# Kernel optimization log

Measured on AMD Instinct MI355X. Metric: run time of the kernel, lower is better.

Reference implementation:

```python
import jax, jax.numpy as jnp
import numpy as np

N = 262144
HIDDEN = 512
NUM_GATES = 64
NUM_GRAPHS = 1024
EPS = 1e-16


def setup_inputs() -> dict:
    key = jax.random.key(0)
    k1, k2, k3 = jax.random.split(key, 3)
    x = jax.random.normal(k1, (N, HIDDEN), dtype=jnp.float32)
    batch = jnp.sort(jax.random.randint(k2, (N,), 0, NUM_GRAPHS, dtype=jnp.int64))
    # Xavier-uniform init for the gate weight [hidden, num_gates]
    limit = float(np.sqrt(6.0 / (HIDDEN + NUM_GATES)))
    W = jax.random.uniform(k3, (HIDDEN, NUM_GATES), dtype=jnp.float32,
                           minval=-limit, maxval=limit)
    return {"x": x, "batch": batch, "W": W}


def _segment_softmax(gate, batch, num_segments):
    # Numerically-stable softmax within each segment (per gate column).
    seg_max = jax.ops.segment_max(gate, batch, num_segments=num_segments)  # [G, num_gates]
    gate = jnp.exp(gate - seg_max[batch])
    seg_sum = jax.ops.segment_sum(gate, batch, num_segments=num_segments)  # [G, num_gates]
    return gate / (seg_sum[batch] + EPS)


def reference(x, batch, W):
    # gate = x @ W : [N, num_gates]
    gate = x @ W
    gate = _segment_softmax(gate, batch, NUM_GRAPHS)
    # weighted scatter-add pooling: out[g] = sum_{i in g} mean_k(gate[i,k]) * x[i]
    weights = jnp.mean(gate, axis=-1, keepdims=True)  # [N, 1]
    out = jax.ops.segment_sum(weights * x, batch, num_segments=NUM_GRAPHS)  # [G, hidden]
    return out
```

## Files before the change

kernel.cpp:

```cpp
#include <hip/hip_runtime.h>

#define NROWS   262144
#define HIDDEN  512
#define NGATES  64
#define NGRAPHS 1024
#define CHUNK   512

typedef __attribute__((ext_vector_type(8))) short short8;
typedef __attribute__((ext_vector_type(4))) float floatx4;

__device__ __forceinline__ unsigned short f2bf(float f) {
    unsigned int u = __float_as_uint(f);
    unsigned int r = (u + 0x7fffu + ((u >> 16) & 1u)) >> 16;
    return (unsigned short)r;
}

__global__ void k_wfrag(const float* __restrict__ W, unsigned short* __restrict__ wf) {
    int tile = blockIdx.x;
    int lane = threadIdx.x;
    int kstep = tile >> 2, nt = tile & 3;
    int kbase = kstep * 32 + (lane >> 4) * 8;
    int col   = nt * 16 + (lane & 15);
    unsigned short* dst = wf + ((size_t)tile * 64 + lane) * 8;
#pragma unroll
    for (int j = 0; j < 8; ++j)
        dst[j] = f2bf(W[(size_t)(kbase + j) * NGATES + col]);
}

__global__ void k_bounds(const int* __restrict__ batch, int* __restrict__ segstart) {
    int g = blockIdx.x * blockDim.x + threadIdx.x;
    if (g > NGRAPHS) return;
    if (g == NGRAPHS) { segstart[g] = NROWS; return; }
    int lo = 0, hi = NROWS;
    while (lo < hi) { int mid = (lo + hi) >> 1; if (batch[mid] < g) lo = mid + 1; else hi = mid; }
    segstart[g] = lo;
}

__global__ __launch_bounds__(256) void k_gemm(const float* __restrict__ x,
                                              const unsigned short* __restrict__ wf,
                                              float* __restrict__ gate) {
    const int t = threadIdx.x;
    const int lane = t & 63, wv = t >> 6;
    const int rowbase = (blockIdx.x * 4 + wv) * 16;
    const int m = lane & 15, q = lane >> 4;
    const float* xrow = x + (size_t)(rowbase + m) * HIDDEN + q * 8;
    const short8* wfv = (const short8*)wf;

    floatx4 acc0 = {0.f,0.f,0.f,0.f}, acc1 = {0.f,0.f,0.f,0.f};
    floatx4 acc2 = {0.f,0.f,0.f,0.f}, acc3 = {0.f,0.f,0.f,0.f};

#pragma unroll 4
    for (int ks = 0; ks < 16; ++ks) {
        float4 a0 = *(const float4*)(xrow + ks * 32);
        float4 a1 = *(const float4*)(xrow + ks * 32 + 4);
        short8 af;
        af[0] = (short)f2bf(a0.x); af[1] = (short)f2bf(a0.y);
        af[2] = (short)f2bf(a0.z); af[3] = (short)f2bf(a0.w);
        af[4] = (short)f2bf(a1.x); af[5] = (short)f2bf(a1.y);
        af[6] = (short)f2bf(a1.z); af[7] = (short)f2bf(a1.w);
        short8 b0 = wfv[(ks * 4 + 0) * 64 + lane];
        short8 b1 = wfv[(ks * 4 + 1) * 64 + lane];
        short8 b2 = wfv[(ks * 4 + 2) * 64 + lane];
        short8 b3 = wfv[(ks * 4 + 3) * 64 + lane];
        acc0 = __builtin_amdgcn_mfma_f32_16x16x32_bf16(af, b0, acc0, 0, 0, 0);
        acc1 = __builtin_amdgcn_mfma_f32_16x16x32_bf16(af, b1, acc1, 0, 0, 0);
        acc2 = __builtin_amdgcn_mfma_f32_16x16x32_bf16(af, b2, acc2, 0, 0, 0);
        acc3 = __builtin_amdgcn_mfma_f32_16x16x32_bf16(af, b3, acc3, 0, 0, 0);
    }

    const int orow = rowbase + q * 4;
    float* gbase = gate + (size_t)orow * NGATES + m;
#pragma unroll
    for (int r = 0; r < 4; ++r) {
        gbase[r * NGATES +  0] = acc0[r];
        gbase[r * NGATES + 16] = acc1[r];
        gbase[r * NGATES + 32] = acc2[r];
        gbase[r * NGATES + 48] = acc3[r];
    }
}

__global__ __launch_bounds__(256) void k_pool(const float* __restrict__ x,
                                              const float* __restrict__ gate,
                                              const int* __restrict__ segstart,
                                              float* __restrict__ out) {
    __shared__ float red[4 * 64];
    __shared__ float mk[64];
    __shared__ float rinv[64];
    __shared__ float wl[CHUNK];

    const int g = blockIdx.x;
    const int t = threadIdx.x;
    const int lane = t & 63, wv = t >> 6;
    const int s = segstart[g], e = segstart[g + 1];

    float mloc = -3.402823466e38f;
    for (int i = s + wv; i < e; i += 4)
        mloc = fmaxf(mloc, gate[(size_t)i * NGATES + lane]);
    red[wv * 64 + lane] = mloc;
    __syncthreads();
    if (t < 64)
        mk[t] = fmaxf(fmaxf(red[t], red[64 + t]), fmaxf(red[128 + t], red[192 + t]));
    __syncthreads();

    const float mkk = mk[lane];
    float sloc = 0.f;
    for (int i = s + wv; i < e; i += 4)
        sloc += __expf(gate[(size_t)i * NGATES + lane] - mkk);
    red[wv * 64 + lane] = sloc;
    __syncthreads();
    if (t < 64)
        rinv[t] = 1.0f / (red[t] + red[64 + t] + red[128 + t] + red[192 + t] + 1e-16f);
    __syncthreads();

    const float rk = rinv[lane];
    const int h0 = t * 2;
    float accx = 0.f, accy = 0.f;

    for (int cbase = s; cbase < e; cbase += CHUNK) {
        const int cn = min(CHUNK, e - cbase);
        for (int i = wv; i < cn; i += 4) {
            const int row = cbase + i;
            float ev = __expf(gate[(size_t)row * NGATES + lane] - mkk) * rk;
#pragma unroll
            for (int off = 32; off >= 1; off >>= 1)
                ev += __shfl_xor(ev, off, 64);
            if (lane == 0) wl[i] = ev * (1.0f / 64.0f);
        }
        __syncthreads();
        for (int i = 0; i < cn; ++i) {
            const float w = wl[i];
            const float2 xv = *(const float2*)(x + (size_t)(cbase + i) * HIDDEN + h0);
            accx = fmaf(w, xv.x, accx);
            accy = fmaf(w, xv.y, accy);
        }
        __syncthreads();
    }

    float2 o; o.x = accx; o.y = accy;
    *(float2*)(out + (size_t)g * HIDDEN + h0) = o;
}

extern "C" void kernel_launch(void* const* d_in, const int* in_sizes, int n_in,
                              void* d_out, int out_size, void* d_ws, size_t ws_size,
                              hipStream_t stream) {
    const float* x     = (const float*)d_in[0];
    const int*   batch = (const int*)d_in[1];
    const float* W     = (const float*)d_in[2];
    float* out = (float*)d_out;

    unsigned short* wfrag = (unsigned short*)d_ws;
    int* segstart = (int*)((char*)d_ws + (64 << 10));
    float* gate   = (float*)((char*)d_ws + (72 << 10));

    hipLaunchKernelGGL(k_wfrag, dim3(64), dim3(64), 0, stream, W, wfrag);
    hipLaunchKernelGGL(k_bounds, dim3(5), dim3(256), 0, stream, batch, segstart);
    hipLaunchKernelGGL(k_gemm, dim3(NROWS / 64), dim3(256), 0, stream, x, wfrag, gate);
    hipLaunchKernelGGL(k_pool, dim3(NGRAPHS), dim3(256), 0, stream, x, gate, segstart, out);
}
```

Measured before the change: 874.1 us.

## Fuse exp and segment-sum into gate GEMM, store bf16 exp, drop max pass

```diff
diff --git a/kernel.cpp b/kernel.cpp
--- a/kernel.cpp
+++ b/kernel.cpp
@@ -13,6 +13,9 @@
     unsigned int u = __float_as_uint(f);
     unsigned int r = (u + 0x7fffu + ((u >> 16) & 1u)) >> 16;
     return (unsigned short)r;
+}
+__device__ __forceinline__ float bf2f(unsigned short u) {
+    return __uint_as_float((unsigned int)u << 16);
 }
 
 __global__ void k_wfrag(const float* __restrict__ W, unsigned short* __restrict__ wf) {
@@ -27,18 +30,24 @@
         dst[j] = f2bf(W[(size_t)(kbase + j) * NGATES + col]);
 }
 
-__global__ void k_bounds(const int* __restrict__ batch, int* __restrict__ segstart) {
-    int g = blockIdx.x * blockDim.x + threadIdx.x;
-    if (g > NGRAPHS) return;
-    if (g == NGRAPHS) { segstart[g] = NROWS; return; }
-    int lo = 0, hi = NROWS;
-    while (lo < hi) { int mid = (lo + hi) >> 1; if (batch[mid] < g) lo = mid + 1; else hi = mid; }
-    segstart[g] = lo;
-}
-
-__global__ __launch_bounds__(256) void k_gemm(const float* __restrict__ x,
+__global__ void k_init(const int* __restrict__ batch, int* __restrict__ segstart,
+                       float* __restrict__ sums) {
+    int tid = blockIdx.x * blockDim.x + threadIdx.x;
+    if (tid < NGRAPHS * NGATES) sums[tid] = 0.f;
+    if (tid <= NGRAPHS) {
+        if (tid == NGRAPHS) { segstart[tid] = NROWS; return; }
+        int lo = 0, hi = NROWS;
+        while (lo < hi) { int mid = (lo + hi) >> 1; if (batch[mid] < tid) lo = mid + 1; else hi = mid; }
+        segstart[tid] = lo;
+    }
+}
+
+__global__ __launch_bounds__(256) void k_gate(const float* __restrict__ x,
                                               const unsigned short* __restrict__ wf,
-                                              float* __restrict__ gate) {
+                                              const int* __restrict__ batch,
+                                              unsigned short* __restrict__ eout,
+                                              float* __restrict__ sums) {
+    __shared__ float red[4][64];
     const int t = threadIdx.x;
     const int lane = t & 63, wv = t >> 6;
     const int rowbase = (blockIdx.x * 4 + wv) * 16;
@@ -68,23 +77,70 @@
         acc3 = __builtin_amdgcn_mfma_f32_16x16x32_bf16(af, b3, acc3, 0, 0, 0);
     }
 
+    float e0[4], e1[4], e2[4], e3[4];
+#pragma unroll
+    for (int r = 0; r < 4; ++r) {
+        e0[r] = __expf(acc0[r]); e1[r] = __expf(acc1[r]);
+        e2[r] = __expf(acc2[r]); e3[r] = __expf(acc3[r]);
+    }
+
     const int orow = rowbase + q * 4;
-    float* gbase = gate + (size_t)orow * NGATES + m;
+    unsigned short* ebase = eout + (size_t)orow * NGATES + m;
 #pragma unroll
     for (int r = 0; r < 4; ++r) {
-        gbase[r * NGATES +  0] = acc0[r];
-        gbase[r * NGATES + 16] = acc1[r];
-        gbase[r * NGATES + 32] = acc2[r];
-        gbase[r * NGATES + 48] = acc3[r];
+        ebase[r * NGATES +  0] = f2bf(e0[r]);
+        ebase[r * NGATES + 16] = f2bf(e1[r]);
+        ebase[r * NGATES + 32] = f2bf(e2[r]);
+        ebase[r * NGATES + 48] = f2bf(e3[r]);
+    }
+
+    const int brow0 = blockIdx.x * 64;
+    const bool uni = (batch[brow0] == batch[brow0 + 63]);
+    if (uni) {
+        float v0 = e0[0]+e0[1]+e0[2]+e0[3];
+        float v1 = e1[0]+e1[1]+e1[2]+e1[3];
+        float v2 = e2[0]+e2[1]+e2[2]+e2[3];
+        float v3 = e3[0]+e3[1]+e3[2]+e3[3];
+        v0 += __shfl_xor(v0, 16, 64); v0 += __shfl_xor(v0, 32, 64);
+        v1 += __shfl_xor(v1, 16, 64); v1 += __shfl_xor(v1, 32, 64);
+        v2 += __shfl_xor(v2, 16, 64); v2 += __shfl_xor(v2, 32, 64);
+        v3 += __shfl_xor(v3, 16, 64); v3 += __shfl_xor(v3, 32, 64);
+        if (q == 0) {
+            red[wv][m]      = v0;
+            red[wv][m + 16] = v1;
+            red[wv][m + 32] = v2;
+            red[wv][m + 48] = v3;
+        }
+        __syncthreads();
+        if (t < 64) {
+            float s = red[0][t] + red[1][t] + red[2][t] + red[3][t];
+            atomicAdd(&sums[(size_t)batch[brow0] * NGATES + t], s);
+        }
+    } else {
+        int b_prev = batch[orow];
+        float a0 = e0[0], a1 = e1[0], a2 = e2[0], a3 = e3[0];
+#pragma unroll
+        for (int r = 1; r < 4; ++r) {
+            int b = batch[orow + r];
+            if (b != b_prev) {
+                float* sb = sums + (size_t)b_prev * NGATES + m;
+                atomicAdd(sb +  0, a0); atomicAdd(sb + 16, a1);
+                atomicAdd(sb + 32, a2); atomicAdd(sb + 48, a3);
+                a0 = a1 = a2 = a3 = 0.f; b_prev = b;
+            }
+            a0 += e0[r]; a1 += e1[r]; a2 += e2[r]; a3 += e3[r];
+        }
+        float* sb = sums + (size_t)b_prev * NGATES + m;
+        atomicAdd(sb +  0, a0); atomicAdd(sb + 16, a1);
+        atomicAdd(sb + 32, a2); atomicAdd(sb + 48, a3);
     }
 }
 
 __global__ __launch_bounds__(256) void k_pool(const float* __restrict__ x,
-                                              const float* __restrict__ gate,
+                                              const unsigned short* __restrict__ eglob,
                                               const int* __restrict__ segstart,
+                                              const float* __restrict__ sums,
                                               float* __restrict__ out) {
-    __shared__ float red[4 * 64];
-    __shared__ float mk[64];
     __shared__ float rinv[64];
     __shared__ float wl[CHUNK];
 
@@ -93,23 +149,7 @@
     const int lane = t & 63, wv = t >> 6;
     const int s = segstart[g], e = segstart[g + 1];
 
-    float mloc = -3.402823466e38f;
-    for (int i = s + wv; i < e; i += 4)
-        mloc = fmaxf(mloc, gate[(size_t)i * NGATES + lane]);
-    red[wv * 64 + lane] = mloc;
-    __syncthreads();
-    if (t < 64)
-        mk[t] = fmaxf(fmaxf(red[t], red[64 + t]), fmaxf(red[128 + t], red[192 + t]));
-    __syncthreads();
-
-    const float mkk = mk[lane];
-    float sloc = 0.f;
-    for (int i = s + wv; i < e; i += 4)
-        sloc += __expf(gate[(size_t)i * NGATES + lane] - mkk);
-    red[wv * 64 + lane] = sloc;
-    __syncthreads();
-    if (t < 64)
-        rinv[t] = 1.0f / (red[t] + red[64 + t] + red[128 + t] + red[192 + t] + 1e-16f);
+    if (t < 64) rinv[t] = 1.0f / (sums[(size_t)g * NGATES + t] + 1e-16f);
     __syncthreads();
 
     const float rk = rinv[lane];
@@ -119,14 +159,14 @@
     for (int cbase = s; cbase < e; cbase += CHUNK) {
         const int cn = min(CHUNK, e - cbase);
         for (int i = wv; i < cn; i += 4) {
-            const int row = cbase + i;
-            float ev = __expf(gate[(size_t)row * NGATES + lane] - mkk) * rk;
+            float ev = bf2f(eglob[(size_t)(cbase + i) * NGATES + lane]) * rk;
 #pragma unroll
             for (int off = 32; off >= 1; off >>= 1)
                 ev += __shfl_xor(ev, off, 64);
             if (lane == 0) wl[i] = ev * (1.0f / 64.0f);
         }
         __syncthreads();
+#pragma unroll 4
         for (int i = 0; i < cn; ++i) {
             const float w = wl[i];
             const float2 xv = *(const float2*)(x + (size_t)(cbase + i) * HIDDEN + h0);
@@ -150,10 +190,11 @@
 
     unsigned short* wfrag = (unsigned short*)d_ws;
     int* segstart = (int*)((char*)d_ws + (64 << 10));
-    float* gate   = (float*)((char*)d_ws + (72 << 10));
+    float* sums   = (float*)((char*)d_ws + (72 << 10));
+    unsigned short* eglob = (unsigned short*)((char*)d_ws + (1 << 20));
 
     hipLaunchKernelGGL(k_wfrag, dim3(64), dim3(64), 0, stream, W, wfrag);
-    hipLaunchKernelGGL(k_bounds, dim3(5), dim3(256), 0, stream, batch, segstart);
-    hipLaunchKernelGGL(k_gemm, dim3(NROWS / 64), dim3(256), 0, stream, x, wfrag, gate);
-    hipLaunchKernelGGL(k_pool, dim3(NGRAPHS), dim3(256), 0, stream, x, gate, segstart, out);
-}
+    hipLaunchKernelGGL(k_init, dim3(256), dim3(256), 0, stream, batch, segstart, sums);
+    hipLaunchKernelGGL(k_gate, dim3(NROWS / 64), dim3(256), 0, stream, x, wfrag, batch, eglob, sums);
+    hipLaunchKernelGGL(k_pool, dim3(NGRAPHS), dim3(256), 0, stream, x, eglob, segstart, sums, out);
+}
```

After: 846.0 us. 3.2% less time.

## Fuse gate GEMM, segment softmax and pooling into one per-graph kernel

Applied to the files above, without the earlier changes.

```diff
diff --git a/kernel.cpp b/kernel.cpp
--- a/kernel.cpp
+++ b/kernel.cpp
@@ -4,7 +4,7 @@
 #define HIDDEN  512
 #define NGATES  64
 #define NGRAPHS 1024
-#define CHUNK   512
+#define MAXR    512
 
 typedef __attribute__((ext_vector_type(8))) short short8;
 typedef __attribute__((ext_vector_type(4))) float floatx4;
@@ -13,6 +13,9 @@
     unsigned int u = __float_as_uint(f);
     unsigned int r = (u + 0x7fffu + ((u >> 16) & 1u)) >> 16;
     return (unsigned short)r;
+}
+__device__ __forceinline__ float bf2f(unsigned short u) {
+    return __uint_as_float((unsigned int)u << 16);
 }
 
 __global__ void k_wfrag(const float* __restrict__ W, unsigned short* __restrict__ wf) {
@@ -36,108 +39,126 @@
     segstart[g] = lo;
 }
 
-__global__ __launch_bounds__(256) void k_gemm(const float* __restrict__ x,
-                                              const unsigned short* __restrict__ wf,
-                                              float* __restrict__ gate) {
-    const int t = threadIdx.x;
-    const int lane = t & 63, wv = t >> 6;
-    const int rowbase = (blockIdx.x * 4 + wv) * 16;
-    const int m = lane & 15, q = lane >> 4;
-    const float* xrow = x + (size_t)(rowbase + m) * HIDDEN + q * 8;
-    const short8* wfv = (const short8*)wf;
-
-    floatx4 acc0 = {0.f,0.f,0.f,0.f}, acc1 = {0.f,0.f,0.f,0.f};
-    floatx4 acc2 = {0.f,0.f,0.f,0.f}, acc3 = {0.f,0.f,0.f,0.f};
-
-#pragma unroll 4
-    for (int ks = 0; ks < 16; ++ks) {
-        float4 a0 = *(const float4*)(xrow + ks * 32);
-        float4 a1 = *(const float4*)(xrow + ks * 32 + 4);
-        short8 af;
-        af[0] = (short)f2bf(a0.x); af[1] = (short)f2bf(a0.y);
-        af[2] = (short)f2bf(a0.z); af[3] = (short)f2bf(a0.w);
-        af[4] = (short)f2bf(a1.x); af[5] = (short)f2bf(a1.y);
-        af[6] = (short)f2bf(a1.z); af[7] = (short)f2bf(a1.w);
-        short8 b0 = wfv[(ks * 4 + 0) * 64 + lane];
-        short8 b1 = wfv[(ks * 4 + 1) * 64 + lane];
-        short8 b2 = wfv[(ks * 4 + 2) * 64 + lane];
-        short8 b3 = wfv[(ks * 4 + 3) * 64 + lane];
-        acc0 = __builtin_amdgcn_mfma_f32_16x16x32_bf16(af, b0, acc0, 0, 0, 0);
-        acc1 = __builtin_amdgcn_mfma_f32_16x16x32_bf16(af, b1, acc1, 0, 0, 0);
-        acc2 = __builtin_amdgcn_mfma_f32_16x16x32_bf16(af, b2, acc2, 0, 0, 0);
-        acc3 = __builtin_amdgcn_mfma_f32_16x16x32_bf16(af, b3, acc3, 0, 0, 0);
-    }
-
-    const int orow = rowbase + q * 4;
-    float* gbase = gate + (size_t)orow * NGATES + m;
-#pragma unroll
-    for (int r = 0; r < 4; ++r) {
-        gbase[r * NGATES +  0] = acc0[r];
-        gbase[r * NGATES + 16] = acc1[r];
-        gbase[r * NGATES + 32] = acc2[r];
-        gbase[r * NGATES + 48] = acc3[r];
-    }
-}
-
-__global__ __launch_bounds__(256) void k_pool(const float* __restrict__ x,
-                                              const float* __restrict__ gate,
-                                              const int* __restrict__ segstart,
-                                              float* __restrict__ out) {
-    __shared__ float red[4 * 64];
-    __shared__ float mk[64];
-    __shared__ float rinv[64];
-    __shared__ float wl[CHUNK];
+__global__ __launch_bounds__(1024, 4) void k_main(const float* __restrict__ x,
+                                                  const unsigned short* __restrict__ wf,
+                                                  const int* __restrict__ segstart,
+                                                  float* __restrict__ out) {
+    __shared__ unsigned short eL[MAXR * NGATES];
+    __shared__ float wl[MAXR];
+    __shared__ float sums[NGATES];
+    __shared__ float rinv[NGATES];
 
     const int g = blockIdx.x;
     const int t = threadIdx.x;
     const int lane = t & 63, wv = t >> 6;
+    const int m = lane & 15, q = lane >> 4;
     const int s = segstart[g], e = segstart[g + 1];
+    const int rows = min(e - s, MAXR);
+    const int tiles = (rows + 15) >> 4;
 
-    float mloc = -3.402823466e38f;
-    for (int i = s + wv; i < e; i += 4)
-        mloc = fmaxf(mloc, gate[(size_t)i * NGATES + lane]);
-    red[wv * 64 + lane] = mloc;
-    __syncthreads();
-    if (t < 64)
-        mk[t] = fmaxf(fmaxf(red[t], red[64 + t]), fmaxf(red[128 + t], red[192 + t]));
+    if (t < NGATES) sums[t] = 0.f;
     __syncthreads();
 
-    const float mkk = mk[lane];
-    float sloc = 0.f;
-    for (int i = s + wv; i < e; i += 4)
-        sloc += __expf(gate[(size_t)i * NGATES + lane] - mkk);
-    red[wv * 64 + lane] = sloc;
+    const short8* wfv = (const short8*)wf;
+    float vs0 = 0.f, vs1 = 0.f, vs2 = 0.f, vs3 = 0.f;
+
+    for (int tile = wv; tile < tiles; tile += 16) {
+        const int garow = s + tile * 16 + m;
+        const float* xrow = x + (size_t)min(garow, NROWS - 1) * HIDDEN + q * 8;
+
+        floatx4 acc0 = {0.f,0.f,0.f,0.f}, acc1 = {0.f,0.f,0.f,0.f};
+        floatx4 acc2 = {0.f,0.f,0.f,0.f}, acc3 = {0.f,0.f,0.f,0.f};
+#pragma unroll 4
+        for (int ks = 0; ks < 16; ++ks) {
+            float4 a0 = *(const float4*)(xrow + ks * 32);
+            float4 a1 = *(const float4*)(xrow + ks * 32 + 4);
+            short8 af;
+            af[0] = (short)f2bf(a0.x); af[1] = (short)f2bf(a0.y);
+            af[2] = (short)f2bf(a0.z); af[3] = (short)f2bf(a0.w);
+            af[4] = (short)f2bf(a1.x); af[5] = (short)f2bf(a1.y);
+            af[6] = (short)f2bf(a1.z); af[7] = (short)f2bf(a1.w);
+            short8 b0 = wfv[(ks * 4 + 0) * 64 + lane];
+            short8 b1 = wfv[(ks * 4 + 1) * 64 + lane];
+            short8 b2 = wfv[(ks * 4 + 2) * 64 + lane];
+            short8 b3 = wfv[(ks * 4 + 3) * 64 + lane];
+            acc0 = __builtin_amdgcn_mfma_f32_16x16x32_bf16(af, b0, acc0, 0, 0, 0);
+            acc1 = __builtin_amdgcn_mfma_f32_16x16x32_bf16(af, b1, acc1, 0, 0, 0);
+            acc2 = __builtin_amdgcn_mfma_f32_16x16x32_bf16(af, b2, acc2, 0, 0, 0);
+            acc3 = __builtin_amdgcn_mfma_f32_16x16x32_bf16(af, b3, acc3, 0, 0, 0);
+        }
+
+        const int rl0 = tile * 16 + q * 4;
+#pragma unroll
+        for (int r = 0; r < 4; ++r) {
+            const int rloc = rl0 + r;
+            const bool valid = rloc < rows;
+            const float e0 = valid ? __expf(acc0[r]) : 0.f;
+            const float e1 = valid ? __expf(acc1[r]) : 0.f;
+            const float e2 = valid ? __expf(acc2[r]) : 0.f;
+            const float e3 = valid ? __expf(acc3[r]) : 0.f;
+            if (valid) {
+                unsigned short* eb = eL + rloc * NGATES + m;
+                eb[ 0] = f2bf(e0); eb[16] = f2bf(e1);
+                eb[32] = f2bf(e2); eb[48] = f2bf(e3);
+            }
+            vs0 += e0; vs1 += e1; vs2 += e2; vs3 += e3;
+        }
+    }
+    vs0 += __shfl_xor(vs0, 16, 64); vs0 += __shfl_xor(vs0, 32, 64);
+    vs1 += __shfl_xor(vs1, 16, 64); vs1 += __shfl_xor(vs1, 32, 64);
+    vs2 += __shfl_xor(vs2, 16, 64); vs2 += __shfl_xor(vs2, 32, 64);
+    vs3 += __shfl_xor(vs3, 16, 64); vs3 += __shfl_xor(vs3, 32, 64);
+    if (q == 0) {
+        atomicAdd(&sums[m],      vs0); atomicAdd(&sums[m + 16], vs1);
+        atomicAdd(&sums[m + 32], vs2); atomicAdd(&sums[m + 48], vs3);
+    }
     __syncthreads();
-    if (t < 64)
-        rinv[t] = 1.0f / (red[t] + red[64 + t] + red[128 + t] + red[192 + t] + 1e-16f);
+    if (t < NGATES) rinv[t] = 1.0f / (sums[t] + 1e-16f);
     __syncthreads();
 
     const float rk = rinv[lane];
-    const int h0 = t * 2;
-    float accx = 0.f, accy = 0.f;
+    const int nrq = (rows + 3) >> 2;
+    for (int i4 = wv; i4 < nrq; i4 += 16) {
+        const int rb = i4 * 4;
+        float v0 = bf2f(eL[(rb + 0) * NGATES + lane]) * rk;
+        float v1 = bf2f(eL[(rb + 1) * NGATES + lane]) * rk;
+        float v2 = bf2f(eL[(rb + 2) * NGATES + lane]) * rk;
+        float v3 = bf2f(eL[(rb + 3) * NGATES + lane]) * rk;
+#pragma unroll
+        for (int off = 1; off < 64; off <<= 1) {
+            v0 += __shfl_xor(v0, off, 64);
+            v1 += __shfl_xor(v1, off, 64);
+            v2 += __shfl_xor(v2, off, 64);
+            v3 += __shfl_xor(v3, off, 64);
+        }
+        if (lane == 0) {
+            wl[rb + 0] = v0 * (1.0f / 64.0f); wl[rb + 1] = v1 * (1.0f / 64.0f);
+            wl[rb + 2] = v2 * (1.0f / 64.0f); wl[rb + 3] = v3 * (1.0f / 64.0f);
+        }
+    }
+    __syncthreads();
 
-    for (int cbase = s; cbase < e; cbase += CHUNK) {
-        const int cn = min(CHUNK, e - cbase);
-        for (int i = wv; i < cn; i += 4) {
-            const int row = cbase + i;
-            float ev = __expf(gate[(size_t)row * NGATES + lane] - mkk) * rk;
-#pragma unroll
-            for (int off = 32; off >= 1; off >>= 1)
-                ev += __shfl_xor(ev, off, 64);
-            if (lane == 0) wl[i] = ev * (1.0f / 64.0f);
-        }
-        __syncthreads();
-        for (int i = 0; i < cn; ++i) {
-            const float w = wl[i];
-            const float2 xv = *(const float2*)(x + (size_t)(cbase + i) * HIDDEN + h0);
-            accx = fmaf(w, xv.x, accx);
-            accy = fmaf(w, xv.y, accy);
-        }
-        __syncthreads();
+    const int h2 = (t & 255) * 2;
+    const int p = t >> 8;
+    float ax = 0.f, ay = 0.f;
+#pragma unroll 4
+    for (int i = p; i < rows; i += 4) {
+        const float w = wl[i];
+        const float2 xv = *(const float2*)(x + (size_t)(s + i) * HIDDEN + h2);
+        ax = fmaf(w, xv.x, ax);
+        ay = fmaf(w, xv.y, ay);
     }
-
-    float2 o; o.x = accx; o.y = accy;
-    *(float2*)(out + (size_t)g * HIDDEN + h0) = o;
+    float* red = (float*)eL;
+    red[(p * 256 + (t & 255)) * 2 + 0] = ax;
+    red[(p * 256 + (t & 255)) * 2 + 1] = ay;
+    __syncthreads();
+    if (p == 0) {
+        const int c = (t & 255) * 2;
+        float2 o;
+        o.x = red[c]     + red[512 + c]     + red[1024 + c]     + red[1536 + c];
+        o.y = red[c + 1] + red[512 + c + 1] + red[1024 + c + 1] + red[1536 + c + 1];
+        *(float2*)(out + (size_t)g * HIDDEN + h2) = o;
+    }
 }
 
 extern "C" void kernel_launch(void* const* d_in, const int* in_sizes, int n_in,
@@ -150,10 +171,8 @@
 
     unsigned short* wfrag = (unsigned short*)d_ws;
     int* segstart = (int*)((char*)d_ws + (64 << 10));
-    float* gate   = (float*)((char*)d_ws + (72 << 10));
 
     hipLaunchKernelGGL(k_wfrag, dim3(64), dim3(64), 0, stream, W, wfrag);
     hipLaunchKernelGGL(k_bounds, dim3(5), dim3(256), 0, stream, batch, segstart);
-    hipLaunchKernelGGL(k_gemm, dim3(NROWS / 64), dim3(256), 0, stream, x, wfrag, gate);
-    hipLaunchKernelGGL(k_pool, dim3(NGRAPHS), dim3(256), 0, stream, x, gate, segstart, out);
+    hipLaunchKernelGGL(k_main, dim3(NGRAPHS), dim3(1024), 0, stream, x, wfrag, segstart, out);
 }
```

New measurement: 777.4 us. 1.12x faster.
